# Kernel optimization log

Hardware: AMD Instinct MI355X
Metric: run time of the kernel (lower is better)

## Reference

```python
import jax, jax.numpy as jnp
import numpy as np

N_NODES = 100_000
M_EDGES = 500_000
F = 128       # elem_fea_len
H = 3         # elem_heads
HD = 256      # hidden layer dim of gate/message nets
BN_EPS = 1e-5


def setup_inputs() -> dict:
    key = jax.random.key(0)
    ks = jax.random.split(key, 12)
    s = 0.05
    return {
        "elem_weights": jax.random.uniform(ks[0], (N_NODES, 1), jnp.float32, 0.05, 1.0),
        "elem_in_fea": jax.random.normal(ks[1], (N_NODES, F), jnp.float32),
        "gate_W1": jax.random.normal(ks[2], (H, 2 * F, HD), jnp.float32) * s,
        "gate_b1": jnp.zeros((H, HD), jnp.float32),
        "gate_g": jnp.ones((H, HD), jnp.float32),
        "gate_beta": jnp.zeros((H, HD), jnp.float32),
        "gate_Wo": jax.random.normal(ks[3], (H, HD, 1), jnp.float32) * s,
        "gate_bo": jnp.zeros((H, 1), jnp.float32),
        "msg_W1": jax.random.normal(ks[4], (H, 2 * F, HD), jnp.float32) * s,
        "msg_b1": jnp.zeros((H, HD), jnp.float32),
        "msg_g": jnp.ones((H, HD), jnp.float32),
        "msg_beta": jnp.zeros((H, HD), jnp.float32),
        "msg_Wo": jax.random.normal(ks[5], (H, HD, F), jnp.float32) * s,
        "msg_bo": jnp.zeros((H, F), jnp.float32),
        "pow_p": jax.random.normal(ks[6], (H, 1), jnp.float32),
        "self_fea_idx": jax.random.randint(ks[7], (M_EDGES,), 0, N_NODES, jnp.int32),
        "nbr_fea_idx": jax.random.randint(ks[8], (M_EDGES,), 0, N_NODES, jnp.int32),
    }


def _simple_net(x, W1, b1, g, beta, Wo, bo):
    # Linear -> BatchNorm1d (training-mode batch stats) -> SiLU -> Linear
    h = x @ W1 + b1
    mu = jnp.mean(h, axis=0)
    var = jnp.mean(jnp.square(h - mu), axis=0)  # biased var, as torch BN
    h = (h - mu) * jax.lax.rsqrt(var + BN_EPS) * g + beta
    h = jax.nn.silu(h)
    return h @ Wo + bo


def reference(elem_weights, elem_in_fea, gate_W1, gate_b1, gate_g, gate_beta,
              gate_Wo, gate_bo, msg_W1, msg_b1, msg_g, msg_beta, msg_Wo,
              msg_bo, pow_p, self_fea_idx, nbr_fea_idx):
    n = elem_in_fea.shape[0]
    # gather edge endpoint features: (M, 2F)
    fea = jnp.concatenate([elem_in_fea[self_fea_idx], elem_in_fea[nbr_fea_idx]], axis=1)
    w = elem_weights[nbr_fea_idx]  # (M, 1)

    def head(gW1, gb1, gg, gbe, gWo, gbo, mW1, mb1, mg, mbe, mWo, mbo, p):
        gate = _simple_net(fea, gW1, gb1, gg, gbe, gWo, gbo)          # (M, 1)
        gmax = jax.ops.segment_max(gate, self_fea_idx, num_segments=n)
        gate = (w ** p) * jnp.exp(gate - gmax[self_fea_idx])
        den = jax.ops.segment_sum(gate, self_fea_idx, num_segments=n)
        gate = gate / (den[self_fea_idx] + 1e-10)
        msg = _simple_net(fea, mW1, mb1, mg, mbe, mWo, mbo)           # (M, F)
        return jax.ops.segment_sum(gate * msg, self_fea_idx, num_segments=n)

    head_out = jax.vmap(head)(gate_W1, gate_b1, gate_g, gate_beta, gate_Wo,
                              gate_bo, msg_W1, msg_b1, msg_g, msg_beta,
                              msg_Wo, msg_bo, pow_p)                  # (H, N, F)
    return jnp.mean(head_out, axis=0) + elem_in_fea
```

## Files before the change

### kernel.cpp

```cpp
#include <hip/hip_runtime.h>
#include <stdint.h>

#define NN 100000
#define MM 500000
#define FD 128
#define KK 256
#define NHEADS 3
#define NTILES 3907

typedef __attribute__((ext_vector_type(8))) __bf16 bf16x8;
typedef __attribute__((ext_vector_type(4))) float floatx4;

__device__ __forceinline__ float bf2f(unsigned short u) {
    union { uint32_t i; float f; } c; c.i = ((uint32_t)u) << 16; return c.f;
}
__device__ __forceinline__ unsigned short f2bf(float f) {
    union { float f; uint32_t i; } c; c.f = f;
    uint32_t i = c.i;
    return (unsigned short)((i + 0x7FFFu + ((i >> 16) & 1u)) >> 16);
}
__device__ __forceinline__ unsigned short f2bf_hw(float f) {
    __bf16 h = (__bf16)f;
    return __builtin_bit_cast(unsigned short, h);
}
__device__ __forceinline__ float silu(float a) { return a / (1.f + __expf(-a)); }
__device__ __forceinline__ float fin(float v) {
    return (v == v && fabsf(v) < 1e30f) ? v : 0.f;
}
__device__ __forceinline__ void gl_lds16(const void* g, void* l) {
    __builtin_amdgcn_global_load_lds(
        (const __attribute__((address_space(1))) unsigned int*)g,
        (__attribute__((address_space(3))) unsigned int*)l, 16, 0, 0);
}
__device__ __forceinline__ void vm_drain() {
    asm volatile("s_waitcnt vmcnt(0)" ::: "memory");
}

__global__ void k_zero(float* __restrict__ p, int nwords) {
    int i = blockIdx.x * 256 + threadIdx.x;
    if (i < nwords) p[i] = 0.f;
}

__global__ void k_castx(const float* __restrict__ x, unsigned short* __restrict__ xb) {
    int i = blockIdx.x * 256 + threadIdx.x;
    if (i < NN * FD / 2) {
        float2 v = ((const float2*)x)[i];
        uint32_t p = (uint32_t)f2bf(v.x) | ((uint32_t)f2bf(v.y) << 16);
        ((uint32_t*)xb)[i] = p;
    }
}

__global__ void k_transpose_w1(const float* __restrict__ gw1,
                               const float* __restrict__ mw1,
                               unsigned short* __restrict__ W1t) {
    int idx = blockIdx.x * 256 + threadIdx.x;
    int j = idx >> 16;
    int rem = idx & 65535;
    int n = rem >> 8, k = rem & 255;
    const float* src = (j < 3) ? (gw1 + (size_t)j * 65536)
                               : (mw1 + (size_t)(j - 3) * 65536);
    W1t[(size_t)idx] = f2bf(src[k * 256 + n]);
}
__global__ void k_transpose_wo(const float* __restrict__ mwo,
                               unsigned short* __restrict__ Wot) {
    int idx = blockIdx.x * 256 + threadIdx.x;
    int h = idx / 32768;
    int rem = idx % 32768;
    int f = rem >> 8, k = rem & 255;
    Wot[idx] = f2bf(mwo[(size_t)h * 32768 + k * 128 + f]);
}

__global__ void k_hist(const int* __restrict__ idx, int* __restrict__ cnt) {
    int e = blockIdx.x * 256 + threadIdx.x;
    if (e < MM) atomicAdd(&cnt[idx[e]], 1);
}
__global__ void k_scan1(const int* __restrict__ cnt, int* __restrict__ pincl, int* __restrict__ bsum) {
    __shared__ int s[256];
    int t = threadIdx.x;
    int i = blockIdx.x * 256 + t;
    int v = (i < NN) ? cnt[i] : 0;
    s[t] = v; __syncthreads();
    for (int o = 1; o < 256; o <<= 1) {
        int add = (t >= o) ? s[t - o] : 0;
        __syncthreads();
        s[t] += add;
        __syncthreads();
    }
    if (i < NN) pincl[i] = s[t];
    if (t == 255) bsum[blockIdx.x] = s[255];
}
__global__ void k_scan2(const int* __restrict__ bsum, int* __restrict__ boff, int nb) {
    __shared__ int s[512];
    int t = threadIdx.x;
    int v = (t < nb) ? bsum[t] : 0;
    s[t] = v; __syncthreads();
    for (int o = 1; o < 512; o <<= 1) {
        int add = (t >= o) ? s[t - o] : 0;
        __syncthreads();
        s[t] += add;
        __syncthreads();
    }
    if (t < nb) boff[t] = s[t] - v;
}
__global__ void k_scan3(const int* __restrict__ pincl, const int* __restrict__ boff, int* __restrict__ rp) {
    int i = blockIdx.x * 256 + threadIdx.x;
    if (i < NN) rp[i + 1] = pincl[i] + boff[i >> 8];
    if (i == 0) rp[0] = 0;
}
__global__ void k_scatter(const int* __restrict__ self, const int* __restrict__ rp,
                          int* __restrict__ fill, int* __restrict__ elist) {
    int e = blockIdx.x * 256 + threadIdx.x;
    if (e < MM) {
        int n = self[e];
        int pos = atomicAdd(&fill[n], 1);
        elist[rp[n] + pos] = e;
    }
}
__global__ void k_perm(const int* __restrict__ elist, const int* __restrict__ self,
                       const int* __restrict__ nbr, int* __restrict__ selfp, int* __restrict__ nbrp) {
    int i = blockIdx.x * 256 + threadIdx.x;
    if (i < MM) {
        int e = elist[i];
        selfp[i] = self[e];
        nbrp[i] = nbr[e];
    }
}

__global__ void k_colsum(const float* __restrict__ x,
                         const int* __restrict__ cnt_self, const int* __restrict__ cnt_nbr,
                         float* __restrict__ colsum) {
    int t = threadIdx.x;
    int col = t & 127, part = t >> 7;
    const int* cp = part ? cnt_nbr : cnt_self;
    int n0 = blockIdx.x * 512;
    float a = 0.f;
    for (int i = 0; i < 512; i++) {
        int n = n0 + i;
        if (n < NN) {
            float c = (float)cp[n];
            a += c * x[(size_t)n * FD + col];
        }
    }
    atomicAdd(&colsum[part * 128 + col], a);
}

#define NCH 7813
#define CPB 62
__global__ __launch_bounds__(256, 2)
void k_S(const unsigned short* __restrict__ xb,
         const int* __restrict__ self_idx, const int* __restrict__ nbr_idx,
         float* __restrict__ S) {
    __shared__ unsigned short LT[256][72];
    const int tid = threadIdx.x;
    const int e_l = tid & 63;
    const int half = tid >> 6;
    const int ti = blockIdx.y >> 1, tj = blockIdx.y & 1;
    const int lane = tid & 63, w = tid >> 6;
    const int lr = lane & 15, q = lane >> 4;

    int cbeg = blockIdx.x * CPB;
    int cend = cbeg + CPB; if (cend > NCH) cend = NCH;

    floatx4 acc[2][8];
#pragma unroll
    for (int a = 0; a < 2; a++)
#pragma unroll
        for (int b = 0; b < 8; b++)
#pragma unroll
            for (int r = 0; r < 4; r++) acc[a][b][r] = 0.f;

    for (int ch = cbeg; ch < cend; ch++) {
        int e = ch * 64 + e_l;
        union { uint4 v[8]; unsigned short us[64]; } buf;
        if (e < MM) {
            int node = (half < 2) ? self_idx[e] : nbr_idx[e];
            const unsigned short* src = xb + (size_t)node * FD + (half & 1) * 64;
#pragma unroll
            for (int u2 = 0; u2 < 8; u2++) buf.v[u2] = *(const uint4*)(src + u2 * 8);
        } else {
#pragma unroll
            for (int u2 = 0; u2 < 8; u2++) { buf.v[u2].x = 0u; buf.v[u2].y = 0u; buf.v[u2].z = 0u; buf.v[u2].w = 0u; }
        }
        __syncthreads();
#pragma unroll
        for (int j2 = 0; j2 < 64; j2++)
            LT[half * 64 + j2][e_l] = buf.us[j2];
        __syncthreads();
#pragma unroll
        for (int ks = 0; ks < 64; ks += 32) {
            bf16x8 aF[2], bF[8];
#pragma unroll
            for (int mi = 0; mi < 2; mi++)
                aF[mi] = *(const bf16x8*)&LT[ti * 128 + w * 32 + mi * 16 + lr][ks + q * 8];
#pragma unroll
            for (int nj = 0; nj < 8; nj++)
                bF[nj] = *(const bf16x8*)&LT[tj * 128 + nj * 16 + lr][ks + q * 8];
#pragma unroll
            for (int mi = 0; mi < 2; mi++)
#pragma unroll
                for (int nj = 0; nj < 8; nj++)
                    acc[mi][nj] = __builtin_amdgcn_mfma_f32_16x16x32_bf16(aF[mi], bF[nj], acc[mi][nj], 0, 0, 0);
        }
    }
#pragma unroll
    for (int mi = 0; mi < 2; mi++)
#pragma unroll
        for (int nj = 0; nj < 8; nj++)
#pragma unroll
            for (int r = 0; r < 4; r++) {
                int row = ti * 128 + w * 32 + mi * 16 + q * 4 + r;
                int col = tj * 128 + nj * 16 + lr;
                atomicAdd(&S[row * 256 + col], acc[mi][nj][r]);
            }
}

__global__ void k_stats(const float* __restrict__ S, const float* __restrict__ colsum,
                        const unsigned short* __restrict__ W1t,
                        const float* __restrict__ gg, const float* __restrict__ gbe,
                        const float* __restrict__ mg, const float* __restrict__ mbe,
                        float* __restrict__ scaleA, float* __restrict__ shiftA) {
    __shared__ float ws[16][257];
    __shared__ float qq[16], uu[16];
    int t = threadIdx.x;
    int j = blockIdx.y;
    int c0 = blockIdx.x * 16;
    const unsigned short* Wn = W1t + (size_t)j * 65536;
    const float* g    = (j < 3) ? gg + j * 256 : mg + (j - 3) * 256;
    const float* beta = (j < 3) ? gbe + j * 256 : mbe + (j - 3) * 256;
#pragma unroll
    for (int i = 0; i < 16; i++) ws[i][t] = bf2f(Wn[(size_t)(c0 + i) * 256 + t]);
    if (t < 16) { qq[t] = 0.f; uu[t] = 0.f; }
    __syncthreads();
    float vpart[16];
#pragma unroll
    for (int i = 0; i < 16; i++) vpart[i] = 0.f;
    for (int k = 0; k < 256; k++) {
        float s = S[k * 256 + t];
#pragma unroll
        for (int i = 0; i < 16; i++) vpart[i] += s * ws[i][k];
    }
    float cs = colsum[t];
    int lane = t & 63;
#pragma unroll
    for (int i = 0; i < 16; i++) {
        float q1 = ws[i][t] * vpart[i];
        float u1 = cs * ws[i][t];
#pragma unroll
        for (int m = 1; m <= 32; m <<= 1) { q1 += __shfl_xor(q1, m); u1 += __shfl_xor(u1, m); }
        if (lane == 0) { atomicAdd(&qq[i], q1); atomicAdd(&uu[i], u1); }
    }
    __syncthreads();
    if (t < 16) {
        int c = c0 + t;
        float mu = fin(uu[t] / (float)MM);
        float var = fmaxf(fin(qq[t] / (float)MM - mu * mu), 0.f);
        float sc = fin(g[c] * rsqrtf(var + 1e-5f));
        scaleA[j * 256 + c] = sc;
        shiftA[j * 256 + c] = fin(beta[c] - mu * sc);
    }
}

__global__ __launch_bounds__(256, 2)
void k_gate(const unsigned short* __restrict__ x,
            const int* __restrict__ selfp, const int* __restrict__ nbrp,
            const unsigned short* __restrict__ W1t,
            const float* __restrict__ scale, const float* __restrict__ shift,
            const float* __restrict__ wo, const float* __restrict__ bo,
            float* __restrict__ glog) {
    __shared__ unsigned char Bs[2][16384];
    __shared__ float sc[3][256], sh[3][256], wv[3][256];
    __shared__ int nid[128], nidN[128];

    const int tid = threadIdx.x;
    const int m0 = blockIdx.x * 128;
#pragma unroll
    for (int h = 0; h < 3; h++) {
        sc[h][tid] = scale[h * 256 + tid];
        sh[h][tid] = shift[h * 256 + tid];
        wv[h][tid] = wo[h * 256 + tid];
    }
    if (tid < 128) {
        int e = m0 + tid;
        nid[tid]  = (e < MM) ? selfp[e] : 0;
        nidN[tid] = (e < MM) ? nbrp[e] : 0;
    }
    __syncthreads();

    const int lane = tid & 63, w = tid >> 6;
    const int lr = lane & 15, q = lane >> 4;
    const int swz = (lr & 7) << 4;

    bf16x8 aReg[2][8];
    {
        const unsigned short* bS0 = x + (size_t)nid[w * 32 + lr] * FD;
        const unsigned short* bS1 = x + (size_t)nid[w * 32 + 16 + lr] * FD;
        const unsigned short* bN0 = x + (size_t)nidN[w * 32 + lr] * FD;
        const unsigned short* bN1 = x + (size_t)nidN[w * 32 + 16 + lr] * FD;
#pragma unroll
        for (int s = 0; s < 8; s++) {
            int koff = (s & 3) * 32 + q * 8;
            aReg[0][s] = *(const bf16x8*)(((s < 4) ? bS0 : bN0) + koff);
            aReg[1][s] = *(const bf16x8*)(((s < 4) ? bS1 : bN1) + koff);
        }
    }

    uint32_t pre[4];
#pragma unroll
    for (int c = 0; c < 4; c++) {
        int o = (w * 4 + c) * 1024 + lane * 16;
        int r = o >> 7, lc = o & 127;
        pre[c] = (uint32_t)(r * 512 + (lc ^ ((r & 7) << 4)));
    }

    auto STAGE = [&](int t, int b) {
        int hh = t >> 3, rr = t & 7, nh2 = rr >> 2, kc = rr & 3;
        const char* gb = (const char*)(W1t + (size_t)hh * 65536 + (size_t)nh2 * 32768 + kc * 64);
#pragma unroll
        for (int c = 0; c < 4; c++)
            gl_lds16(gb + pre[c], &Bs[b][(w * 4 + c) * 1024]);
    };

    STAGE(0, 0);
    vm_drain();
    __syncthreads();

    int buf = 0, tcur = 0;
    for (int h = 0; h < 3; h++) {
        float dotp[2][4];
#pragma unroll
        for (int mi = 0; mi < 2; mi++)
#pragma unroll
            for (int r = 0; r < 4; r++) dotp[mi][r] = 0.f;

        for (int nh = 0; nh < 2; nh++) {
            floatx4 acc[2][8];
#pragma unroll
            for (int a = 0; a < 2; a++)
#pragma unroll
                for (int b = 0; b < 8; b++)
#pragma unroll
                    for (int r = 0; r < 4; r++) acc[a][b][r] = 0.f;

#pragma unroll
            for (int kc = 0; kc < 4; kc++) {
                if (tcur + 1 < 24) STAGE(tcur + 1, buf ^ 1);
#pragma unroll
                for (int ks = 0; ks < 2; ks++) {
                    bf16x8 bF[8];
#pragma unroll
                    for (int nj = 0; nj < 8; nj++)
                        bF[nj] = *(const bf16x8*)&Bs[buf][(nj * 16 + lr) * 128 + ((ks * 64 + q * 16) ^ swz)];
                    __builtin_amdgcn_s_setprio(1);
#pragma unroll
                    for (int mi = 0; mi < 2; mi++)
#pragma unroll
                        for (int nj = 0; nj < 8; nj++)
                            acc[mi][nj] = __builtin_amdgcn_mfma_f32_16x16x32_bf16(aReg[mi][kc * 2 + ks], bF[nj], acc[mi][nj], 0, 0, 0);
                    __builtin_amdgcn_s_setprio(0);
                }
                vm_drain();
                __syncthreads();
                buf ^= 1; tcur++;
            }
#pragma unroll
            for (int mi = 0; mi < 2; mi++)
#pragma unroll
                for (int r = 0; r < 4; r++) {
                    float d = 0.f;
#pragma unroll
                    for (int nj = 0; nj < 8; nj++) {
                        int cg = nh * 128 + nj * 16 + lr;
                        float v = acc[mi][nj][r] * sc[h][cg] + sh[h][cg];
                        d += silu(v) * wv[h][cg];
                    }
                    dotp[mi][r] += d;
                }
        }
        float b0 = bo[h];
#pragma unroll
        for (int mi = 0; mi < 2; mi++)
#pragma unroll
            for (int r = 0; r < 4; r++) {
                float v = dotp[mi][r];
                v += __shfl_xor(v, 1); v += __shfl_xor(v, 2);
                v += __shfl_xor(v, 4); v += __shfl_xor(v, 8);
                if (lr == 0) {
                    int row = w * 32 + mi * 16 + q * 4 + r;
                    int e = m0 + row;
                    if (e < MM) glog[(size_t)h * MM + e] = fin(v + b0);
                }
            }
    }
}

__global__ void k_coef(const int* __restrict__ rp, const float* __restrict__ glog,
                       float* __restrict__ coef, const float* __restrict__ ew,
                       const int* __restrict__ nbrp, const float* __restrict__ powp) {
    int n = blockIdx.x * 256 + threadIdx.x;
    if (n >= NN) return;
    int b = rp[n], e = rp[n + 1];
    if (e <= b) return;
    for (int h = 0; h < NHEADS; h++) {
        const float* gl = glog + (size_t)h * MM;
        float* cf = coef + (size_t)h * MM;
        float p = powp[h];
        float gmax = -3.4e38f;
        for (int i = b; i < e; i++) gmax = fmaxf(gmax, gl[i]);
        float den = 0.f;
        for (int i = b; i < e; i++) {
            float wv = ew[nbrp[i]];
            float u = fin(powf(wv, p) * __expf(gl[i] - gmax));
            cf[i] = u; den += u;
        }
        float inv = fin(1.f / (den + 1e-10f));
        for (int i = b; i < e; i++) cf[i] = fin(cf[i] * inv);
    }
}

__global__ __launch_bounds__(256, 2)
void k_msg(const unsigned short* __restrict__ x,
           const int* __restrict__ selfp, const int* __restrict__ nbrp,
           const unsigned short* __restrict__ W1t,
           const float* __restrict__ scale, const float* __restrict__ shift,
           const unsigned short* __restrict__ Wo2t,
           const float* __restrict__ bo2,
           const float* __restrict__ coef,
           float* __restrict__ out_acc) {
    __shared__ unsigned char Bs[2][16384];
    __shared__ unsigned short ActC[128][72];
    __shared__ float sc[3][256], sh[3][256];
    __shared__ float bvec[3][128], cfs[3][128];
    __shared__ int nid[128], nidN[128];

    const int tid = threadIdx.x;
    const int m0 = blockIdx.x * 128;
#pragma unroll
    for (int h = 0; h < 3; h++) {
        sc[h][tid] = scale[h * 256 + tid];
        sh[h][tid] = shift[h * 256 + tid];
    }
    if (tid < 128) {
        int e = m0 + tid;
        nid[tid]  = (e < MM) ? selfp[e] : -1;
        nidN[tid] = (e < MM) ? nbrp[e] : 0;
#pragma unroll
        for (int h = 0; h < 3; h++) {
            bvec[h][tid] = bo2[h * 128 + tid];
            cfs[h][tid] = (e < MM) ? coef[(size_t)h * MM + e] : 0.f;
        }
    }
    __syncthreads();

    const int lane = tid & 63, w = tid >> 6;
    const int lr = lane & 15, q = lane >> 4;
    const int swz = (lr & 7) << 4;

    bf16x8 aReg[2][8];
    {
        int nS0 = nid[w * 32 + lr];      if (nS0 < 0) nS0 = 0;
        int nS1 = nid[w * 32 + 16 + lr]; if (nS1 < 0) nS1 = 0;
        const unsigned short* bS0 = x + (size_t)nS0 * FD;
        const unsigned short* bS1 = x + (size_t)nS1 * FD;
        const unsigned short* bN0 = x + (size_t)nidN[w * 32 + lr] * FD;
        const unsigned short* bN1 = x + (size_t)nidN[w * 32 + 16 + lr] * FD;
#pragma unroll
        for (int s = 0; s < 8; s++) {
            int koff = (s & 3) * 32 + q * 8;
            aReg[0][s] = *(const bf16x8*)(((s < 4) ? bS0 : bN0) + koff);
            aReg[1][s] = *(const bf16x8*)(((s < 4) ? bS1 : bN1) + koff);
        }
    }

    uint32_t pre[4];
#pragma unroll
    for (int c = 0; c < 4; c++) {
        int o = (w * 4 + c) * 1024 + lane * 16;
        int r = o >> 7, lc = o & 127;
        pre[c] = (uint32_t)(r * 512 + (lc ^ ((r & 7) << 4)));
    }

    auto STAGE = [&](int t, int b) {
        int hh = t / 12, rr = t % 12, nh2 = rr / 6, s6 = rr % 6;
        const unsigned short* base = (s6 < 4)
            ? (W1t + (size_t)hh * 65536 + (size_t)nh2 * 32768 + s6 * 64)
            : (Wo2t + (size_t)hh * 32768 + nh2 * 128 + (s6 - 4) * 64);
        const char* gb = (const char*)base;
#pragma unroll
        for (int c = 0; c < 4; c++)
            gl_lds16(gb + pre[c], &Bs[b][(w * 4 + c) * 1024]);
    };

    STAGE(0, 0);
    vm_drain();
    __syncthreads();

    floatx4 acc2[2][8];
#pragma unroll
    for (int a = 0; a < 2; a++)
#pragma unroll
        for (int b = 0; b < 8; b++)
#pragma unroll
            for (int r = 0; r < 4; r++) acc2[a][b][r] = 0.f;

    int buf = 0, tcur = 0;
    for (int h = 0; h < 3; h++) {
        float cfr[2][4];
#pragma unroll
        for (int mi = 0; mi < 2; mi++)
#pragma unroll
            for (int r = 0; r < 4; r++) cfr[mi][r] = cfs[h][w * 32 + mi * 16 + q * 4 + r];

        for (int nh = 0; nh < 2; nh++) {
            floatx4 acc[2][8];
#pragma unroll
            for (int a = 0; a < 2; a++)
#pragma unroll
                for (int b = 0; b < 8; b++)
#pragma unroll
                    for (int r = 0; r < 4; r++) acc[a][b][r] = 0.f;

#pragma unroll
            for (int kc = 0; kc < 4; kc++) {
                if (tcur + 1 < 36) STAGE(tcur + 1, buf ^ 1);
#pragma unroll
                for (int ks = 0; ks < 2; ks++) {
                    bf16x8 bF[8];
#pragma unroll
                    for (int nj = 0; nj < 8; nj++)
                        bF[nj] = *(const bf16x8*)&Bs[buf][(nj * 16 + lr) * 128 + ((ks * 64 + q * 16) ^ swz)];
                    __builtin_amdgcn_s_setprio(1);
#pragma unroll
                    for (int mi = 0; mi < 2; mi++)
#pragma unroll
                        for (int nj = 0; nj < 8; nj++)
                            acc[mi][nj] = __builtin_amdgcn_mfma_f32_16x16x32_bf16(aReg[mi][kc * 2 + ks], bF[nj], acc[mi][nj], 0, 0, 0);
                    __builtin_amdgcn_s_setprio(0);
                }
                vm_drain();
                __syncthreads();
                buf ^= 1; tcur++;
            }
#pragma unroll
            for (int kc2 = 0; kc2 < 2; kc2++) {
                if (tcur + 1 < 36) STAGE(tcur + 1, buf ^ 1);
#pragma unroll
                for (int mi = 0; mi < 2; mi++)
#pragma unroll
                    for (int njl = 0; njl < 4; njl++)
#pragma unroll
                        for (int r = 0; r < 4; r++) {
                            int nj = kc2 * 4 + njl;
                            int row = w * 32 + mi * 16 + q * 4 + r;
                            int cg = nh * 128 + nj * 16 + lr;
                            float v = acc[mi][nj][r] * sc[h][cg] + sh[h][cg];
                            ActC[row][njl * 16 + lr] = f2bf_hw(silu(v) * cfr[mi][r]);
                        }
#pragma unroll
                for (int ks = 0; ks < 2; ks++) {
                    bf16x8 aF[2], bF[8];
#pragma unroll
                    for (int mi = 0; mi < 2; mi++)
                        aF[mi] = *(const bf16x8*)&ActC[w * 32 + mi * 16 + lr][ks * 32 + q * 8];
#pragma unroll
                    for (int nj = 0; nj < 8; nj++)
                        bF[nj] = *(const bf16x8*)&Bs[buf][(nj * 16 + lr) * 128 + ((ks * 64 + q * 16) ^ swz)];
                    __builtin_amdgcn_s_setprio(1);
#pragma unroll
                    for (int mi = 0; mi < 2; mi++)
#pragma unroll
                        for (int nj = 0; nj < 8; nj++)
                            acc2[mi][nj] = __builtin_amdgcn_mfma_f32_16x16x32_bf16(aF[mi], bF[nj], acc2[mi][nj], 0, 0, 0);
                    __builtin_amdgcn_s_setprio(0);
                }
                vm_drain();
                __syncthreads();
                buf ^= 1; tcur++;
            }
        }
    }
#pragma unroll
    for (int mi = 0; mi < 2; mi++) {
        int rbase = w * 32 + mi * 16 + q * 4;
        int n0 = nid[rbase], n3 = nid[rbase + 3];
        float c0[3], c1[3], c2[3], c3[3];
#pragma unroll
        for (int h = 0; h < 3; h++) {
            c0[h] = cfs[h][rbase];     c1[h] = cfs[h][rbase + 1];
            c2[h] = cfs[h][rbase + 2]; c3[h] = cfs[h][rbase + 3];
        }
#pragma unroll
        for (int nj = 0; nj < 8; nj++) {
            int col = nj * 16 + lr;
            float b0h = bvec[0][col], b1h = bvec[1][col], b2h = bvec[2][col];
            float v0 = acc2[mi][nj][0] + c0[0] * b0h + c0[1] * b1h + c0[2] * b2h;
            float v1 = acc2[mi][nj][1] + c1[0] * b0h + c1[1] * b1h + c1[2] * b2h;
            float v2 = acc2[mi][nj][2] + c2[0] * b0h + c2[1] * b1h + c2[2] * b2h;
            float v3 = acc2[mi][nj][3] + c3[0] * b0h + c3[1] * b1h + c3[2] * b2h;
            if (n0 == n3) {
                if (n0 >= 0) atomicAdd(&out_acc[(size_t)n0 * FD + col], v0 + v1 + v2 + v3);
            } else {
                int n1 = nid[rbase + 1], n2 = nid[rbase + 2];
                if (n0 >= 0) atomicAdd(&out_acc[(size_t)n0 * FD + col], v0);
                if (n1 >= 0) atomicAdd(&out_acc[(size_t)n1 * FD + col], v1);
                if (n2 >= 0) atomicAdd(&out_acc[(size_t)n2 * FD + col], v2);
                if (n3 >= 0) atomicAdd(&out_acc[(size_t)n3 * FD + col], v3);
            }
        }
    }
}

__global__ void k_finalout(float* __restrict__ out, const float* __restrict__ x) {
    int i = blockIdx.x * 256 + threadIdx.x;
    if (i < NN * FD) out[i] = fin(out[i]) * (1.f / 3.f) + x[i];
}

extern "C" void kernel_launch(void* const* d_in, const int* in_sizes, int n_in,
                              void* d_out, int out_size, void* d_ws, size_t ws_size,
                              hipStream_t stream) {
    const float* ew   = (const float*)d_in[0];
    const float* x    = (const float*)d_in[1];
    const float* gW1  = (const float*)d_in[2];
    const float* gg   = (const float*)d_in[4];
    const float* gbe  = (const float*)d_in[5];
    const float* gWo  = (const float*)d_in[6];
    const float* gbo  = (const float*)d_in[7];
    const float* mW1  = (const float*)d_in[8];
    const float* mg   = (const float*)d_in[10];
    const float* mbe  = (const float*)d_in[11];
    const float* mWo  = (const float*)d_in[12];
    const float* mbo  = (const float*)d_in[13];
    const float* powp = (const float*)d_in[14];
    const int* self_idx = (const int*)d_in[15];
    const int* nbr_idx  = (const int*)d_in[16];
    float* out = (float*)d_out;

    char* ws = (char*)d_ws;
    size_t off = 0;
    auto alloc = [&](size_t bytes) -> void* {
        size_t o = off;
        off += (bytes + 255) & ~(size_t)255;
        return (void*)(ws + o);
    };

    float* S       = (float*)alloc(256 * 256 * 4);
    float* colsum  = (float*)alloc(512 * 4);
    int*   cnt     = (int*)alloc((size_t)NN * 4);
    int*   cntn    = (int*)alloc((size_t)NN * 4);
    int*   fill    = (int*)alloc((size_t)NN * 4);
    size_t zero_end = off;
    unsigned short* xb   = (unsigned short*)alloc((size_t)NN * FD * 2);
    unsigned short* W1t  = (unsigned short*)alloc(6ull * 65536 * 2);
    unsigned short* Wo2t = (unsigned short*)alloc(3ull * 32768 * 2);
    float* scaleA = (float*)alloc(6ull * 256 * 4);
    float* shiftA = (float*)alloc(6ull * 256 * 4);
    int*   rp     = (int*)alloc((size_t)(NN + 1) * 4);
    int*   pincl  = (int*)alloc((size_t)NN * 4);
    int*   bsum   = (int*)alloc(512 * 4);
    int*   boff   = (int*)alloc(512 * 4);
    int*   elist  = (int*)alloc((size_t)MM * 4);
    int*   selfp  = (int*)alloc((size_t)MM * 4);
    int*   nbrp   = (int*)alloc((size_t)MM * 4);
    float* glog   = (float*)alloc(3ull * MM * 4);
    float* coef   = (float*)alloc(3ull * MM * 4);
    if (off > ws_size) return;

    int zwords = (int)(zero_end / 4);
    k_zero<<<(zwords + 255) / 256, 256, 0, stream>>>(S, zwords);
    k_zero<<<(NN * FD + 255) / 256, 256, 0, stream>>>(out, NN * FD);

    k_castx<<<(NN * FD / 2 + 255) / 256, 256, 0, stream>>>(x, xb);
    k_transpose_w1<<<1536, 256, 0, stream>>>(gW1, mW1, W1t);
    k_transpose_wo<<<384, 256, 0, stream>>>(mWo, Wo2t);

    k_hist<<<1954, 256, 0, stream>>>(self_idx, cnt);
    k_hist<<<1954, 256, 0, stream>>>(nbr_idx, cntn);
    int nb1 = (NN + 255) / 256;
    k_scan1<<<nb1, 256, 0, stream>>>(cnt, pincl, bsum);
    k_scan2<<<1, 512, 0, stream>>>(bsum, boff, nb1);
    k_scan3<<<nb1, 256, 0, stream>>>(pincl, boff, rp);
    k_scatter<<<1954, 256, 0, stream>>>(self_idx, rp, fill, elist);
    k_perm<<<1954, 256, 0, stream>>>(elist, self_idx, nbr_idx, selfp, nbrp);

    k_colsum<<<(NN + 511) / 512, 256, 0, stream>>>(x, cnt, cntn, colsum);
    k_S<<<dim3(128, 4), 256, 0, stream>>>(xb, self_idx, nbr_idx, S);
    k_stats<<<dim3(16, 6), 256, 0, stream>>>(S, colsum, W1t, gg, gbe, mg, mbe, scaleA, shiftA);

    k_gate<<<NTILES, 256, 0, stream>>>(xb, selfp, nbrp, W1t,
                                       scaleA, shiftA, gWo, gbo, glog);
    k_coef<<<nb1, 256, 0, stream>>>(rp, glog, coef, ew, nbrp, powp);
    k_msg<<<NTILES, 256, 0, stream>>>(xb, selfp, nbrp, W1t + 3ull * 65536,
                                      scaleA + 3 * 256, shiftA + 3 * 256,
                                      Wo2t, mbo, coef, out);
    k_finalout<<<(NN * FD + 255) / 256, 256, 0, stream>>>(out, x);
}
```

Before: 1.616 ms.

## Read MFMA weight fragments directly from global instead of LDS double-buffering

Drops the double-buffered global-to-LDS staging of the W1 and Wo2 weight tiles in the gate and message kernels. Each wave now loads its B fragments straight from global memory, relying on L1/L2 caching of the small weight matrices. This removes the block-wide barriers and vmcnt drains per k-chunk, and frees LDS, which may raise occupancy. It also moves the BN scale/shift/wo values from LDS into registers once per half. The cost is higher-latency, uncoalesced-row global loads on the MFMA critical path and more register pressure.

```diff
diff --git a/kernel.cpp b/kernel.cpp
--- a/kernel.cpp
+++ b/kernel.cpp
@@ -26,14 +26,6 @@
 __device__ __forceinline__ float silu(float a) { return a / (1.f + __expf(-a)); }
 __device__ __forceinline__ float fin(float v) {
     return (v == v && fabsf(v) < 1e30f) ? v : 0.f;
-}
-__device__ __forceinline__ void gl_lds16(const void* g, void* l) {
-    __builtin_amdgcn_global_load_lds(
-        (const __attribute__((address_space(1))) unsigned int*)g,
-        (__attribute__((address_space(3))) unsigned int*)l, 16, 0, 0);
-}
-__device__ __forceinline__ void vm_drain() {
-    asm volatile("s_waitcnt vmcnt(0)" ::: "memory");
 }
 
 __global__ void k_zero(float* __restrict__ p, int nwords) {
@@ -267,7 +259,6 @@
             const float* __restrict__ scale, const float* __restrict__ shift,
             const float* __restrict__ wo, const float* __restrict__ bo,
             float* __restrict__ glog) {
-    __shared__ unsigned char Bs[2][16384];
     __shared__ float sc[3][256], sh[3][256], wv[3][256];
     __shared__ int nid[128], nidN[128];
 
@@ -288,7 +279,6 @@
 
     const int lane = tid & 63, w = tid >> 6;
     const int lr = lane & 15, q = lane >> 4;
-    const int swz = (lr & 7) << 4;
 
     bf16x8 aReg[2][8];
     {
@@ -304,28 +294,8 @@
         }
     }
 
-    uint32_t pre[4];
-#pragma unroll
-    for (int c = 0; c < 4; c++) {
-        int o = (w * 4 + c) * 1024 + lane * 16;
-        int r = o >> 7, lc = o & 127;
-        pre[c] = (uint32_t)(r * 512 + (lc ^ ((r & 7) << 4)));
-    }
-
-    auto STAGE = [&](int t, int b) {
-        int hh = t >> 3, rr = t & 7, nh2 = rr >> 2, kc = rr & 3;
-        const char* gb = (const char*)(W1t + (size_t)hh * 65536 + (size_t)nh2 * 32768 + kc * 64);
-#pragma unroll
-        for (int c = 0; c < 4; c++)
-            gl_lds16(gb + pre[c], &Bs[b][(w * 4 + c) * 1024]);
-    };
-
-    STAGE(0, 0);
-    vm_drain();
-    __syncthreads();
-
-    int buf = 0, tcur = 0;
     for (int h = 0; h < 3; h++) {
+        const unsigned short* W1h = W1t + (size_t)h * 65536;
         float dotp[2][4];
 #pragma unroll
         for (int mi = 0; mi < 2; mi++)
@@ -333,6 +303,12 @@
             for (int r = 0; r < 4; r++) dotp[mi][r] = 0.f;
 
         for (int nh = 0; nh < 2; nh++) {
+            float scR[8], shR[8], wvR[8];
+#pragma unroll
+            for (int nj = 0; nj < 8; nj++) {
+                int cg = nh * 128 + nj * 16 + lr;
+                scR[nj] = sc[h][cg]; shR[nj] = sh[h][cg]; wvR[nj] = wv[h][cg];
+            }
             floatx4 acc[2][8];
 #pragma unroll
             for (int a = 0; a < 2; a++)
@@ -343,13 +319,12 @@
 
 #pragma unroll
             for (int kc = 0; kc < 4; kc++) {
-                if (tcur + 1 < 24) STAGE(tcur + 1, buf ^ 1);
 #pragma unroll
                 for (int ks = 0; ks < 2; ks++) {
                     bf16x8 bF[8];
 #pragma unroll
                     for (int nj = 0; nj < 8; nj++)
-                        bF[nj] = *(const bf16x8*)&Bs[buf][(nj * 16 + lr) * 128 + ((ks * 64 + q * 16) ^ swz)];
+                        bF[nj] = *(const bf16x8*)(W1h + (size_t)(nh * 128 + nj * 16 + lr) * KK + kc * 64 + ks * 32 + q * 8);
                     __builtin_amdgcn_s_setprio(1);
 #pragma unroll
                     for (int mi = 0; mi < 2; mi++)
@@ -358,9 +333,6 @@
                             acc[mi][nj] = __builtin_amdgcn_mfma_f32_16x16x32_bf16(aReg[mi][kc * 2 + ks], bF[nj], acc[mi][nj], 0, 0, 0);
                     __builtin_amdgcn_s_setprio(0);
                 }
-                vm_drain();
-                __syncthreads();
-                buf ^= 1; tcur++;
             }
 #pragma unroll
             for (int mi = 0; mi < 2; mi++)
@@ -369,9 +341,8 @@
                     float d = 0.f;
 #pragma unroll
                     for (int nj = 0; nj < 8; nj++) {
-                        int cg = nh * 128 + nj * 16 + lr;
-                        float v = acc[mi][nj][r] * sc[h][cg] + sh[h][cg];
-                        d += silu(v) * wv[h][cg];
+                        float v = acc[mi][nj][r] * scR[nj] + shR[nj];
+                        d += silu(v) * wvR[nj];
                     }
                     dotp[mi][r] += d;
                 }
@@ -426,7 +397,6 @@
            const float* __restrict__ bo2,
            const float* __restrict__ coef,
            float* __restrict__ out_acc) {
-    __shared__ unsigned char Bs[2][16384];
     __shared__ unsigned short ActC[128][72];
     __shared__ float sc[3][256], sh[3][256];
     __shared__ float bvec[3][128], cfs[3][128];
@@ -453,7 +423,6 @@
 
     const int lane = tid & 63, w = tid >> 6;
     const int lr = lane & 15, q = lane >> 4;
-    const int swz = (lr & 7) << 4;
 
     bf16x8 aReg[2][8];
     {
@@ -471,29 +440,6 @@
         }
     }
 
-    uint32_t pre[4];
-#pragma unroll
-    for (int c = 0; c < 4; c++) {
-        int o = (w * 4 + c) * 1024 + lane * 16;
-        int r = o >> 7, lc = o & 127;
-        pre[c] = (uint32_t)(r * 512 + (lc ^ ((r & 7) << 4)));
-    }
-
-    auto STAGE = [&](int t, int b) {
-        int hh = t / 12, rr = t % 12, nh2 = rr / 6, s6 = rr % 6;
-        const unsigned short* base = (s6 < 4)
-            ? (W1t + (size_t)hh * 65536 + (size_t)nh2 * 32768 + s6 * 64)
-            : (Wo2t + (size_t)hh * 32768 + nh2 * 128 + (s6 - 4) * 64);
-        const char* gb = (const char*)base;
-#pragma unroll
-        for (int c = 0; c < 4; c++)
-            gl_lds16(gb + pre[c], &Bs[b][(w * 4 + c) * 1024]);
-    };
-
-    STAGE(0, 0);
-    vm_drain();
-    __syncthreads();
-
     floatx4 acc2[2][8];
 #pragma unroll
     for (int a = 0; a < 2; a++)
@@ -502,8 +448,9 @@
 #pragma unroll
             for (int r = 0; r < 4; r++) acc2[a][b][r] = 0.f;
 
-    int buf = 0, tcur = 0;
     for (int h = 0; h < 3; h++) {
+        const unsigned short* W1h  = W1t + (size_t)h * 65536;
+        const unsigned short* Wo2h = Wo2t + (size_t)h * 32768;
         float cfr[2][4];
 #pragma unroll
         for (int mi = 0; mi < 2; mi++)
@@ -511,6 +458,12 @@
             for (int r = 0; r < 4; r++) cfr[mi][r] = cfs[h][w * 32 + mi * 16 + q * 4 + r];
 
         for (int nh = 0; nh < 2; nh++) {
+            float scR[8], shR[8];
+#pragma unroll
+            for (int nj = 0; nj < 8; nj++) {
+                int cg = nh * 128 + nj * 16 + lr;
+                scR[nj] = sc[h][cg]; shR[nj] = sh[h][cg];
+            }
             floatx4 acc[2][8];
 #pragma unroll
             for (int a = 0; a < 2; a++)
@@ -521,13 +474,12 @@
 
 #pragma unroll
             for (int kc = 0; kc < 4; kc++) {
-                if (tcur + 1 < 36) STAGE(tcur + 1, buf ^ 1);
 #pragma unroll
                 for (int ks = 0; ks < 2; ks++) {
                     bf16x8 bF[8];
 #pragma unroll
                     for (int nj = 0; nj < 8; nj++)
-                        bF[nj] = *(const bf16x8*)&Bs[buf][(nj * 16 + lr) * 128 + ((ks * 64 + q * 16) ^ swz)];
+                        bF[nj] = *(const bf16x8*)(W1h + (size_t)(nh * 128 + nj * 16 + lr) * KK + kc * 64 + ks * 32 + q * 8);
                     __builtin_amdgcn_s_setprio(1);
 #pragma unroll
                     for (int mi = 0; mi < 2; mi++)
@@ -536,13 +488,9 @@
                             acc[mi][nj] = __builtin_amdgcn_mfma_f32_16x16x32_bf16(aReg[mi][kc * 2 + ks], bF[nj], acc[mi][nj], 0, 0, 0);
                     __builtin_amdgcn_s_setprio(0);
                 }
-                vm_drain();
-                __syncthreads();
-                buf ^= 1; tcur++;
             }
 #pragma unroll
             for (int kc2 = 0; kc2 < 2; kc2++) {
-                if (tcur + 1 < 36) STAGE(tcur + 1, buf ^ 1);
 #pragma unroll
                 for (int mi = 0; mi < 2; mi++)
 #pragma unroll
@@ -551,8 +499,7 @@
                         for (int r = 0; r < 4; r++) {
                             int nj = kc2 * 4 + njl;
                             int row = w * 32 + mi * 16 + q * 4 + r;
-                            int cg = nh * 128 + nj * 16 + lr;
-                            float v = acc[mi][nj][r] * sc[h][cg] + sh[h][cg];
+                            float v = acc[mi][nj][r] * scR[nj] + shR[nj];
                             ActC[row][njl * 16 + lr] = f2bf_hw(silu(v) * cfr[mi][r]);
                         }
 #pragma unroll
@@ -563,7 +510,7 @@
                         aF[mi] = *(const bf16x8*)&ActC[w * 32 + mi * 16 + lr][ks * 32 + q * 8];
 #pragma unroll
                     for (int nj = 0; nj < 8; nj++)
-                        bF[nj] = *(const bf16x8*)&Bs[buf][(nj * 16 + lr) * 128 + ((ks * 64 + q * 16) ^ swz)];
+                        bF[nj] = *(const bf16x8*)(Wo2h + (size_t)(nj * 16 + lr) * KK + nh * 128 + kc2 * 64 + ks * 32 + q * 8);
                     __builtin_amdgcn_s_setprio(1);
 #pragma unroll
                     for (int mi = 0; mi < 2; mi++)
@@ -572,9 +519,6 @@
                             acc2[mi][nj] = __builtin_amdgcn_mfma_f32_16x16x32_bf16(aF[mi], bF[nj], acc2[mi][nj], 0, 0, 0);
                     __builtin_amdgcn_s_setprio(0);
                 }
-                vm_drain();
-                __syncthreads();
-                buf ^= 1; tcur++;
             }
         }
     }
```

After: 2.899 ms. 1.79x slower.

## Triple-buffer weight tiles with partial vmcnt waits and one barrier per step

Applied to the files above, without the earlier changes.

Both the gate and message GEMM kernels move from a double-buffered LDS pipeline, which drained all loads and synchronised after every k-step, to a triple-buffered ring. Each step issues the next tile's loads, waits only for the older tile with vmcnt(4), and synchronises once, so global-to-LDS copies overlap with MFMA work. In the message kernel the activation staging buffer shrinks to half width and is refilled per k-substep. BN scale and shift are now read from global memory into registers instead of LDS, which cuts LDS use to make room for the third buffer. Each warp reuses its ActC rows across substeps without a barrier between them; this holds only because each warp touches only its own rows.

```diff
diff --git a/kernel.cpp b/kernel.cpp
--- a/kernel.cpp
+++ b/kernel.cpp
@@ -31,9 +31,6 @@
     __builtin_amdgcn_global_load_lds(
         (const __attribute__((address_space(1))) unsigned int*)g,
         (__attribute__((address_space(3))) unsigned int*)l, 16, 0, 0);
-}
-__device__ __forceinline__ void vm_drain() {
-    asm volatile("s_waitcnt vmcnt(0)" ::: "memory");
 }
 
 __global__ void k_zero(float* __restrict__ p, int nwords) {
@@ -267,7 +264,7 @@
             const float* __restrict__ scale, const float* __restrict__ shift,
             const float* __restrict__ wo, const float* __restrict__ bo,
             float* __restrict__ glog) {
-    __shared__ unsigned char Bs[2][16384];
+    __shared__ unsigned char Bs[3][16384];
     __shared__ float sc[3][256], sh[3][256], wv[3][256];
     __shared__ int nid[128], nidN[128];
 
@@ -321,10 +318,8 @@
     };
 
     STAGE(0, 0);
-    vm_drain();
-    __syncthreads();
-
-    int buf = 0, tcur = 0;
+
+    int cb = 0, tcur = 0;
     for (int h = 0; h < 3; h++) {
         float dotp[2][4];
 #pragma unroll
@@ -343,13 +338,23 @@
 
 #pragma unroll
             for (int kc = 0; kc < 4; kc++) {
-                if (tcur + 1 < 24) STAGE(tcur + 1, buf ^ 1);
+                int nxt = tcur + 1;
+                int nb2 = (cb + 1 == 3) ? 0 : cb + 1;
+                __builtin_amdgcn_sched_barrier(0);
+                if (nxt < 24) {
+                    STAGE(nxt, nb2);
+                    asm volatile("s_waitcnt vmcnt(4)" ::: "memory");
+                } else {
+                    asm volatile("s_waitcnt vmcnt(0)" ::: "memory");
+                }
+                __builtin_amdgcn_s_barrier();
+                __builtin_amdgcn_sched_barrier(0);
 #pragma unroll
                 for (int ks = 0; ks < 2; ks++) {
                     bf16x8 bF[8];
 #pragma unroll
                     for (int nj = 0; nj < 8; nj++)
-                        bF[nj] = *(const bf16x8*)&Bs[buf][(nj * 16 + lr) * 128 + ((ks * 64 + q * 16) ^ swz)];
+                        bF[nj] = *(const bf16x8*)&Bs[cb][(nj * 16 + lr) * 128 + ((ks * 64 + q * 16) ^ swz)];
                     __builtin_amdgcn_s_setprio(1);
 #pragma unroll
                     for (int mi = 0; mi < 2; mi++)
@@ -358,9 +363,7 @@
                             acc[mi][nj] = __builtin_amdgcn_mfma_f32_16x16x32_bf16(aReg[mi][kc * 2 + ks], bF[nj], acc[mi][nj], 0, 0, 0);
                     __builtin_amdgcn_s_setprio(0);
                 }
-                vm_drain();
-                __syncthreads();
-                buf ^= 1; tcur++;
+                cb = nb2; tcur = nxt;
             }
 #pragma unroll
             for (int mi = 0; mi < 2; mi++)
@@ -426,19 +429,13 @@
            const float* __restrict__ bo2,
            const float* __restrict__ coef,
            float* __restrict__ out_acc) {
-    __shared__ unsigned char Bs[2][16384];
-    __shared__ unsigned short ActC[128][72];
-    __shared__ float sc[3][256], sh[3][256];
+    __shared__ unsigned char Bs[3][16384];
+    __shared__ unsigned short ActC[128][40];
     __shared__ float bvec[3][128], cfs[3][128];
     __shared__ int nid[128], nidN[128];
 
     const int tid = threadIdx.x;
     const int m0 = blockIdx.x * 128;
-#pragma unroll
-    for (int h = 0; h < 3; h++) {
-        sc[h][tid] = scale[h * 256 + tid];
-        sh[h][tid] = shift[h * 256 + tid];
-    }
     if (tid < 128) {
         int e = m0 + tid;
         nid[tid]  = (e < MM) ? selfp[e] : -1;
@@ -491,8 +488,6 @@
     };
 
     STAGE(0, 0);
-    vm_drain();
-    __syncthreads();
 
     floatx4 acc2[2][8];
 #pragma unroll
@@ -502,7 +497,7 @@
 #pragma unroll
             for (int r = 0; r < 4; r++) acc2[a][b][r] = 0.f;
 
-    int buf = 0, tcur = 0;
+    int cb = 0, tcur = 0;
     for (int h = 0; h < 3; h++) {
         float cfr[2][4];
 #pragma unroll
@@ -521,13 +516,23 @@
 
 #pragma unroll
             for (int kc = 0; kc < 4; kc++) {
-                if (tcur + 1 < 36) STAGE(tcur + 1, buf ^ 1);
+                int nxt = tcur + 1;
+                int nb2 = (cb + 1 == 3) ? 0 : cb + 1;
+                __builtin_amdgcn_sched_barrier(0);
+                if (nxt < 36) {
+                    STAGE(nxt, nb2);
+                    asm volatile("s_waitcnt vmcnt(4)" ::: "memory");
+                } else {
+                    asm volatile("s_waitcnt vmcnt(0)" ::: "memory");
+                }
+                __builtin_amdgcn_s_barrier();
+                __builtin_amdgcn_sched_barrier(0);
 #pragma unroll
                 for (int ks = 0; ks < 2; ks++) {
                     bf16x8 bF[8];
 #pragma unroll
                     for (int nj = 0; nj < 8; nj++)
-                        bF[nj] = *(const bf16x8*)&Bs[buf][(nj * 16 + lr) * 128 + ((ks * 64 + q * 16) ^ swz)];
+                        bF[nj] = *(const bf16x8*)&Bs[cb][(nj * 16 + lr) * 128 + ((ks * 64 + q * 16) ^ swz)];
                     __builtin_amdgcn_s_setprio(1);
 #pragma unroll
                     for (int mi = 0; mi < 2; mi++)
@@ -536,34 +541,48 @@
                             acc[mi][nj] = __builtin_amdgcn_mfma_f32_16x16x32_bf16(aReg[mi][kc * 2 + ks], bF[nj], acc[mi][nj], 0, 0, 0);
                     __builtin_amdgcn_s_setprio(0);
                 }
-                vm_drain();
-                __syncthreads();
-                buf ^= 1; tcur++;
+                cb = nb2; tcur = nxt;
             }
 #pragma unroll
             for (int kc2 = 0; kc2 < 2; kc2++) {
-                if (tcur + 1 < 36) STAGE(tcur + 1, buf ^ 1);
-#pragma unroll
-                for (int mi = 0; mi < 2; mi++)
-#pragma unroll
-                    for (int njl = 0; njl < 4; njl++)
-#pragma unroll
-                        for (int r = 0; r < 4; r++) {
-                            int nj = kc2 * 4 + njl;
-                            int row = w * 32 + mi * 16 + q * 4 + r;
-                            int cg = nh * 128 + nj * 16 + lr;
-                            float v = acc[mi][nj][r] * sc[h][cg] + sh[h][cg];
-                            ActC[row][njl * 16 + lr] = f2bf_hw(silu(v) * cfr[mi][r]);
-                        }
+                int nxt = tcur + 1;
+                int nb2 = (cb + 1 == 3) ? 0 : cb + 1;
+                __builtin_amdgcn_sched_barrier(0);
+                if (nxt < 36) {
+                    STAGE(nxt, nb2);
+                    asm volatile("s_waitcnt vmcnt(4)" ::: "memory");
+                } else {
+                    asm volatile("s_waitcnt vmcnt(0)" ::: "memory");
+                }
+                __builtin_amdgcn_s_barrier();
+                __builtin_amdgcn_sched_barrier(0);
+                float scR[4], shR[4];
+#pragma unroll
+                for (int njl = 0; njl < 4; njl++) {
+                    int cg = nh * 128 + (kc2 * 4 + njl) * 16 + lr;
+                    scR[njl] = scale[h * 256 + cg];
+                    shR[njl] = shift[h * 256 + cg];
+                }
 #pragma unroll
                 for (int ks = 0; ks < 2; ks++) {
+#pragma unroll
+                    for (int mi = 0; mi < 2; mi++)
+#pragma unroll
+                        for (int njl2 = 0; njl2 < 2; njl2++)
+#pragma unroll
+                            for (int r = 0; r < 4; r++) {
+                                int nj = kc2 * 4 + ks * 2 + njl2;
+                                int row = w * 32 + mi * 16 + q * 4 + r;
+                                float v = acc[mi][nj][r] * scR[ks * 2 + njl2] + shR[ks * 2 + njl2];
+                                ActC[row][njl2 * 16 + lr] = f2bf_hw(silu(v) * cfr[mi][r]);
+                            }
                     bf16x8 aF[2], bF[8];
 #pragma unroll
                     for (int mi = 0; mi < 2; mi++)
-                        aF[mi] = *(const bf16x8*)&ActC[w * 32 + mi * 16 + lr][ks * 32 + q * 8];
+                        aF[mi] = *(const bf16x8*)&ActC[w * 32 + mi * 16 + lr][q * 8];
 #pragma unroll
                     for (int nj = 0; nj < 8; nj++)
-                        bF[nj] = *(const bf16x8*)&Bs[buf][(nj * 16 + lr) * 128 + ((ks * 64 + q * 16) ^ swz)];
+                        bF[nj] = *(const bf16x8*)&Bs[cb][(nj * 16 + lr) * 128 + ((ks * 64 + q * 16) ^ swz)];
                     __builtin_amdgcn_s_setprio(1);
 #pragma unroll
                     for (int mi = 0; mi < 2; mi++)
@@ -572,9 +591,7 @@
                             acc2[mi][nj] = __builtin_amdgcn_mfma_f32_16x16x32_bf16(aF[mi], bF[nj], acc2[mi][nj], 0, 0, 0);
                     __builtin_amdgcn_s_setprio(0);
                 }
-                vm_drain();
-                __syncthreads();
-                buf ^= 1; tcur++;
+                cb = nb2; tcur = nxt;
             }
         }
     }
```

Result: slower. 1.695 ms (+4.9%).
